# Kernel optimization log

Hardware: AMD Instinct MI355X
Metric: run time of the kernel (lower is better)

## Reference

```python
import jax, jax.numpy as jnp
import numpy as np

N = 8388608      # number of points
S = 32768        # number of superpoints (segments)


def setup_inputs() -> dict:
    key = jax.random.key(0)
    k1, k2, k3 = jax.random.split(key, 3)
    pos = jax.random.normal(k1, (N, 3), dtype=jnp.float32)
    idx = jnp.sort(jax.random.randint(k2, (N,), 0, S, dtype=jnp.int64))
    w = jax.random.uniform(k3, (N,), dtype=jnp.float32)  # non-negative weights
    return {"pos": pos, "idx": idx, "w": w, "num_super": S}


def reference(pos, idx, w, num_super):
    # Per-segment min / max of coordinates: [S, 3]
    mn = jax.ops.segment_min(pos, idx, num_segments=num_super, indices_are_sorted=True)
    mx = jax.ops.segment_max(pos, idx, num_segments=num_super, indices_are_sorted=True)
    # Per-segment diameter = largest coordinate extent: [S]
    diameter_segment = (mx - mn).max(axis=1)
    # Weighted per-segment center: sum(w*pos) / sum(w), guarding zero-weight segments
    w_sum = jax.ops.segment_sum(w, idx, num_segments=num_super, indices_are_sorted=True)
    w_sum_safe = jnp.where(w_sum == 0, 1.0, w_sum)
    center_segment = (
        jax.ops.segment_sum(pos * w[:, None], idx, num_segments=num_super,
                            indices_are_sorted=True)
        / w_sum_safe[:, None]
    )
    # Gather per-node center/diameter and normalize into unit sphere
    pos_out = (pos - center_segment[idx]) / (diameter_segment[idx][:, None] + 0.01)
    return pos_out, diameter_segment.reshape(-1, 1)
```

## Files before the change

kernel.cpp:

```cpp
#include <hip/hip_runtime.h>

#define WAVE 64
#define SPB 4
typedef float v4f __attribute__((ext_vector_type(4)));

__global__ void detect_idx64(const unsigned int* __restrict__ w32, long long N,
                             int* __restrict__ flag) {
    long long base = (N / 2) | 1LL;
    long long stride = ((N / 2) / 64) & ~1LL;
    if (stride < 2) stride = 2;
    long long p = base + (long long)threadIdx.x * stride;
    unsigned int v = (p < N) ? w32[p] : 0u;
    unsigned long long nz = __ballot(v != 0u);
    if (threadIdx.x == 0) *flag = (nz == 0ULL) ? 1 : 0;
}

__device__ __forceinline__ int load_idx(const void* __restrict__ p,
                                        long long i, int is64) {
    return is64 ? (int)((const long long*)p)[i] : ((const int*)p)[i];
}

__global__ void find_bounds(const void* __restrict__ idxp,
                            const int* __restrict__ flag,
                            int* __restrict__ start,
                            long long N, int S) {
    const long long b = ((long long)blockIdx.x * blockDim.x + threadIdx.x) << 2;
    const bool active = b < N;
    const int is64 = *flag;

    int v0 = 0, v1 = 0, v2 = 0, v3 = 0;
    int nval = 0;
    if (active) {
        if (b + 4 <= N) {
            nval = 4;
            if (is64) {
                const longlong2* p = (const longlong2*)((const long long*)idxp + b);
                longlong2 q0 = p[0], q1 = p[1];
                v0 = (int)q0.x; v1 = (int)q0.y; v2 = (int)q1.x; v3 = (int)q1.y;
            } else {
                int4 q = *(const int4*)((const int*)idxp + b);
                v0 = q.x; v1 = q.y; v2 = q.z; v3 = q.w;
            }
        } else {
            nval = (int)(N - b);
            v0 = load_idx(idxp, b, is64);
            if (nval > 1) v1 = load_idx(idxp, b + 1, is64);
            if (nval > 2) v2 = load_idx(idxp, b + 2, is64);
        }
    }
    int last = (nval == 4) ? v3 : (nval == 3) ? v2 : (nval == 2) ? v1 : v0;
    int prev = __shfl_up(last, 1);
    if ((threadIdx.x & 63) == 0)
        prev = (b == 0) ? -1 : (active ? load_idx(idxp, b - 1, is64) : 0);
    if (!active) return;

    int c = prev;
    if (nval >= 1) { if (v0 > c) { for (int t = c + 1; t <= v0; ++t) start[t] = (int)(b);     } c = v0; }
    if (nval >= 2) { if (v1 > c) { for (int t = c + 1; t <= v1; ++t) start[t] = (int)(b + 1); } c = v1; }
    if (nval >= 3) { if (v2 > c) { for (int t = c + 1; t <= v2; ++t) start[t] = (int)(b + 2); } c = v2; }
    if (nval >= 4) { if (v3 > c) { for (int t = c + 1; t <= v3; ++t) start[t] = (int)(b + 3); } c = v3; }
    if (b + nval >= N)
        for (int t = c + 1; t <= S; ++t) start[t] = (int)N;
}

__global__ __launch_bounds__(SPB * WAVE)
void seg_norm(const float* __restrict__ pos,
              const float* __restrict__ w,
              const int* __restrict__ start,
              float* __restrict__ out,
              float* __restrict__ diam_out,
              int S) {
    const int wid  = threadIdx.x >> 6;
    const int lane = threadIdx.x & 63;
    const int step = gridDim.x * SPB;

    const float4* __restrict__ pos4 = (const float4*)pos;
    const float4* __restrict__ w4   = (const float4*)w;
    float4* __restrict__ out4 = (float4*)out;

    for (int s = blockIdx.x * SPB + wid; s < S; s += step) {
        const int su = __builtin_amdgcn_readfirstlane(s);
        const int lo = start[su], hi = start[su + 1];
        const int g0 = lo >> 2, g1 = (hi + 3) >> 2;

        const int ga = g0 + lane;
        const int gb = ga + WAVE;
        const bool va = ga < g1, vb = gb < g1;
        const bool anyb = __any(vb);

        float4 a0 = {0,0,0,0}, a1 = {0,0,0,0}, a2 = {0,0,0,0}, aw = {0,0,0,0};
        float4 b0 = {0,0,0,0}, b1 = {0,0,0,0}, b2 = {0,0,0,0}, bw = {0,0,0,0};
        if (va) {
            a0 = pos4[3LL * ga]; a1 = pos4[3LL * ga + 1]; a2 = pos4[3LL * ga + 2];
            aw = w4[ga];
        }
        if (anyb && vb) {
            b0 = pos4[3LL * gb]; b1 = pos4[3LL * gb + 1]; b2 = pos4[3LL * gb + 2];
            bw = w4[gb];
        }

        float mnx = INFINITY,  mny = INFINITY,  mnz = INFINITY;
        float mxx = -INFINITY, mxy = -INFINITY, mxz = -INFINITY;
        float sw = 0.f, swx = 0.f, swy = 0.f, swz = 0.f;

        #define PROC(PI, X, Y, Z, WV)                                        \
        {                                                                    \
            bool in = ((PI) >= lo) & ((PI) < hi);                            \
            float xv = (X), yv = (Y), zv = (Z);                              \
            float wv = in ? (WV) : 0.f;                                      \
            mnx = fminf(mnx, in ? xv :  INFINITY);                           \
            mxx = fmaxf(mxx, in ? xv : -INFINITY);                           \
            mny = fminf(mny, in ? yv :  INFINITY);                           \
            mxy = fmaxf(mxy, in ? yv : -INFINITY);                           \
            mnz = fminf(mnz, in ? zv :  INFINITY);                           \
            mxz = fmaxf(mxz, in ? zv : -INFINITY);                           \
            sw += wv;                                                        \
            swx = fmaf(wv, xv, swx);                                         \
            swy = fmaf(wv, yv, swy);                                         \
            swz = fmaf(wv, zv, swz);                                         \
        }
        #define PROC_GROUP(G, R0, R1, R2, RW)                                \
        {                                                                    \
            const int p = (G) << 2;                                          \
            PROC(p + 0, R0.x, R0.y, R0.z, RW.x)                              \
            PROC(p + 1, R0.w, R1.x, R1.y, RW.y)                              \
            PROC(p + 2, R1.z, R1.w, R2.x, RW.z)                              \
            PROC(p + 3, R2.y, R2.z, R2.w, RW.w)                              \
        }

        PROC_GROUP(ga, a0, a1, a2, aw)
        if (anyb) PROC_GROUP(gb, b0, b1, b2, bw)

        for (int g = g0 + 2 * WAVE + lane; g < g1; g += WAVE) {
            float4 c0 = pos4[3LL * g], c1 = pos4[3LL * g + 1], c2 = pos4[3LL * g + 2];
            float4 cw = w4[g];
            PROC_GROUP(g, c0, c1, c2, cw)
        }

        #pragma unroll
        for (int off = 1; off < WAVE; off <<= 1) {
            mnx = fminf(mnx, __shfl_xor(mnx, off));
            mny = fminf(mny, __shfl_xor(mny, off));
            mnz = fminf(mnz, __shfl_xor(mnz, off));
            mxx = fmaxf(mxx, __shfl_xor(mxx, off));
            mxy = fmaxf(mxy, __shfl_xor(mxy, off));
            mxz = fmaxf(mxz, __shfl_xor(mxz, off));
            sw  += __shfl_xor(sw,  off);
            swx += __shfl_xor(swx, off);
            swy += __shfl_xor(swy, off);
            swz += __shfl_xor(swz, off);
        }

        const float diam = fmaxf(mxx - mnx, fmaxf(mxy - mny, mxz - mnz));
        const float wsafe = (sw == 0.f) ? 1.f : sw;
        const float cx = swx / wsafe, cy = swy / wsafe, cz = swz / wsafe;
        const float inv = 1.f / (diam + 0.01f);
        if (lane == 0) diam_out[s] = diam;

        #define STORE_GROUP(G, R0, R1, R2)                                       \
        {                                                                        \
            const int p = (G) << 2;                                              \
            float4 ra, rb, rc;                                                   \
            ra.x = (R0.x - cx) * inv; ra.y = (R0.y - cy) * inv;                  \
            ra.z = (R0.z - cz) * inv; ra.w = (R0.w - cx) * inv;                  \
            rb.x = (R1.x - cy) * inv; rb.y = (R1.y - cz) * inv;                  \
            rb.z = (R1.z - cx) * inv; rb.w = (R1.w - cy) * inv;                  \
            rc.x = (R2.x - cz) * inv; rc.y = (R2.y - cx) * inv;                  \
            rc.z = (R2.z - cy) * inv; rc.w = (R2.w - cz) * inv;                  \
            if (p >= lo && p + 4 <= hi) {                                        \
                __builtin_nontemporal_store(*(const v4f*)&ra, (v4f*)&out4[3LL * (G)]);     \
                __builtin_nontemporal_store(*(const v4f*)&rb, (v4f*)&out4[3LL * (G) + 1]); \
                __builtin_nontemporal_store(*(const v4f*)&rc, (v4f*)&out4[3LL * (G) + 2]); \
            } else {                                                             \
                const long long f = 12LL * (G);                                  \
                if (p + 0 >= lo && p + 0 < hi) {                                 \
                    out[f + 0] = ra.x; out[f + 1]  = ra.y; out[f + 2]  = ra.z;   \
                }                                                                \
                if (p + 1 >= lo && p + 1 < hi) {                                 \
                    out[f + 3] = ra.w; out[f + 4]  = rb.x; out[f + 5]  = rb.y;   \
                }                                                                \
                if (p + 2 >= lo && p + 2 < hi) {                                 \
                    out[f + 6] = rb.z; out[f + 7]  = rb.w; out[f + 8]  = rc.x;   \
                }                                                                \
                if (p + 3 >= lo && p + 3 < hi) {                                 \
                    out[f + 9] = rc.y; out[f + 10] = rc.z; out[f + 11] = rc.w;   \
                }                                                                \
            }                                                                    \
        }

        STORE_GROUP(ga, a0, a1, a2)
        if (anyb) STORE_GROUP(gb, b0, b1, b2)

        for (int g = g0 + 2 * WAVE + lane; g < g1; g += WAVE) {
            float4 c0 = pos4[3LL * g], c1 = pos4[3LL * g + 1], c2 = pos4[3LL * g + 2];
            STORE_GROUP(g, c0, c1, c2)
        }

        #undef STORE_GROUP
        #undef PROC_GROUP
        #undef PROC
    }
}

extern "C" void kernel_launch(void* const* d_in, const int* in_sizes, int n_in,
                              void* d_out, int out_size, void* d_ws, size_t ws_size,
                              hipStream_t stream) {
    const float* pos  = (const float*)d_in[0];
    const void*  idxp = d_in[1];
    const float* w    = (const float*)d_in[2];

    const long long N = (long long)in_sizes[0] / 3;
    const int S = out_size - in_sizes[0];

    float* out = (float*)d_out;
    float* diam_out = out + (long long)in_sizes[0];

    int* flag  = (int*)d_ws;
    int* start = (int*)((char*)d_ws + 256);

    detect_idx64<<<1, 64, 0, stream>>>((const unsigned int*)idxp, N, flag);

    const long long nt4 = (N + 3) >> 2;
    find_bounds<<<(int)((nt4 + 255) / 256), 256, 0, stream>>>(idxp, flag, start, N, S);

    int sgrid = (S + SPB - 1) / SPB;
    int grid = sgrid < 2048 ? sgrid : 2048;
    seg_norm<<<grid, SPB * WAVE, 0, stream>>>(pos, w, start, out, diam_out, S);
}
```

Measured before the change: 65.54 us.

## Process two segments per wave to overlap their loads, drop grid-stride loop

Each wave now handles segments sA and sA+H together, issuing the loads for both before any reduction so more memory requests are in flight per wave. The persistent grid-stride loop is replaced by a one-shot grid of H/WPB blocks. Nontemporal stores become plain float4 stores, and the __any guard on the second chunk is removed. The cost is roughly double the register pressure per wave, which may lower occupancy.

```diff
diff --git a/kernel.cpp b/kernel.cpp
--- a/kernel.cpp
+++ b/kernel.cpp
@@ -1,8 +1,7 @@
 #include <hip/hip_runtime.h>
 
 #define WAVE 64
-#define SPB 4
-typedef float v4f __attribute__((ext_vector_type(4)));
+#define WPB 4
 
 __global__ void detect_idx64(const unsigned int* __restrict__ w32, long long N,
                              int* __restrict__ flag) {
@@ -63,143 +62,183 @@
         for (int t = c + 1; t <= S; ++t) start[t] = (int)N;
 }
 
-__global__ __launch_bounds__(SPB * WAVE)
+__global__ __launch_bounds__(WPB * WAVE)
 void seg_norm(const float* __restrict__ pos,
               const float* __restrict__ w,
               const int* __restrict__ start,
               float* __restrict__ out,
               float* __restrict__ diam_out,
-              int S) {
+              int S, int H) {
     const int wid  = threadIdx.x >> 6;
     const int lane = threadIdx.x & 63;
-    const int step = gridDim.x * SPB;
+    const int sA = blockIdx.x * WPB + wid;
+    if (sA >= H) return;
+    const int sB = sA + H;
+    const bool hasB = sB < S;
+
+    const int loA = start[sA], hiA = start[sA + 1];
+    const int loB = hasB ? start[sB] : 0;
+    const int hiB = hasB ? start[sB + 1] : 0;
 
     const float4* __restrict__ pos4 = (const float4*)pos;
     const float4* __restrict__ w4   = (const float4*)w;
+
+    const int g0A = loA >> 2, g1A = (hiA + 3) >> 2;
+    const int g0B = loB >> 2, g1B = (hiB + 3) >> 2;
+    const int gaA = g0A + lane, gbA = gaA + WAVE;
+    const int gaB = g0B + lane, gbB = gaB + WAVE;
+    const bool vaA = gaA < g1A, vbA = gbA < g1A;
+    const bool vaB = gaB < g1B, vbB = gbB < g1B;
+
+    float4 Aa0 = {0,0,0,0}, Aa1 = {0,0,0,0}, Aa2 = {0,0,0,0}, Aaw = {0,0,0,0};
+    float4 Ab0 = {0,0,0,0}, Ab1 = {0,0,0,0}, Ab2 = {0,0,0,0}, Abw = {0,0,0,0};
+    float4 Ba0 = {0,0,0,0}, Ba1 = {0,0,0,0}, Ba2 = {0,0,0,0}, Baw = {0,0,0,0};
+    float4 Bb0 = {0,0,0,0}, Bb1 = {0,0,0,0}, Bb2 = {0,0,0,0}, Bbw = {0,0,0,0};
+    if (vaA) {
+        Aa0 = pos4[3LL * gaA]; Aa1 = pos4[3LL * gaA + 1]; Aa2 = pos4[3LL * gaA + 2];
+        Aaw = w4[gaA];
+    }
+    if (vbA) {
+        Ab0 = pos4[3LL * gbA]; Ab1 = pos4[3LL * gbA + 1]; Ab2 = pos4[3LL * gbA + 2];
+        Abw = w4[gbA];
+    }
+    if (vaB) {
+        Ba0 = pos4[3LL * gaB]; Ba1 = pos4[3LL * gaB + 1]; Ba2 = pos4[3LL * gaB + 2];
+        Baw = w4[gaB];
+    }
+    if (vbB) {
+        Bb0 = pos4[3LL * gbB]; Bb1 = pos4[3LL * gbB + 1]; Bb2 = pos4[3LL * gbB + 2];
+        Bbw = w4[gbB];
+    }
+
+    #define DECL_ACC(P)                                                      \
+        float P##mnx = INFINITY,  P##mny = INFINITY,  P##mnz = INFINITY;     \
+        float P##mxx = -INFINITY, P##mxy = -INFINITY, P##mxz = -INFINITY;    \
+        float P##sw = 0.f, P##swx = 0.f, P##swy = 0.f, P##swz = 0.f;
+    DECL_ACC(A_)
+    DECL_ACC(B_)
+
+    #define PROC(P, PI, LO, HI, X, Y, Z, WV)                                 \
+    {                                                                        \
+        bool in = ((PI) >= (LO)) & ((PI) < (HI));                            \
+        float xv = (X), yv = (Y), zv = (Z);                                  \
+        float wv = in ? (WV) : 0.f;                                          \
+        P##mnx = fminf(P##mnx, in ? xv :  INFINITY);                         \
+        P##mxx = fmaxf(P##mxx, in ? xv : -INFINITY);                         \
+        P##mny = fminf(P##mny, in ? yv :  INFINITY);                         \
+        P##mxy = fmaxf(P##mxy, in ? yv : -INFINITY);                         \
+        P##mnz = fminf(P##mnz, in ? zv :  INFINITY);                         \
+        P##mxz = fmaxf(P##mxz, in ? zv : -INFINITY);                         \
+        P##sw += wv;                                                         \
+        P##swx = fmaf(wv, xv, P##swx);                                       \
+        P##swy = fmaf(wv, yv, P##swy);                                       \
+        P##swz = fmaf(wv, zv, P##swz);                                       \
+    }
+    #define PROC_GROUP(P, G, LO, HI, R0, R1, R2, RW)                         \
+    {                                                                        \
+        const int p_ = (G) << 2;                                             \
+        PROC(P, p_ + 0, LO, HI, R0.x, R0.y, R0.z, RW.x)                      \
+        PROC(P, p_ + 1, LO, HI, R0.w, R1.x, R1.y, RW.y)                      \
+        PROC(P, p_ + 2, LO, HI, R1.z, R1.w, R2.x, RW.z)                      \
+        PROC(P, p_ + 3, LO, HI, R2.y, R2.z, R2.w, RW.w)                      \
+    }
+
+    PROC_GROUP(A_, gaA, loA, hiA, Aa0, Aa1, Aa2, Aaw)
+    PROC_GROUP(A_, gbA, loA, hiA, Ab0, Ab1, Ab2, Abw)
+    PROC_GROUP(B_, gaB, loB, hiB, Ba0, Ba1, Ba2, Baw)
+    PROC_GROUP(B_, gbB, loB, hiB, Bb0, Bb1, Bb2, Bbw)
+
+    for (int g = g0A + 2 * WAVE + lane; g < g1A; g += WAVE) {
+        float4 c0 = pos4[3LL * g], c1 = pos4[3LL * g + 1], c2 = pos4[3LL * g + 2];
+        float4 cw = w4[g];
+        PROC_GROUP(A_, g, loA, hiA, c0, c1, c2, cw)
+    }
+    for (int g = g0B + 2 * WAVE + lane; g < g1B; g += WAVE) {
+        float4 c0 = pos4[3LL * g], c1 = pos4[3LL * g + 1], c2 = pos4[3LL * g + 2];
+        float4 cw = w4[g];
+        PROC_GROUP(B_, g, loB, hiB, c0, c1, c2, cw)
+    }
+
+    #define RED(P)                                                           \
+        P##mnx = fminf(P##mnx, __shfl_xor(P##mnx, off));                     \
+        P##mny = fminf(P##mny, __shfl_xor(P##mny, off));                     \
+        P##mnz = fminf(P##mnz, __shfl_xor(P##mnz, off));                     \
+        P##mxx = fmaxf(P##mxx, __shfl_xor(P##mxx, off));                     \
+        P##mxy = fmaxf(P##mxy, __shfl_xor(P##mxy, off));                     \
+        P##mxz = fmaxf(P##mxz, __shfl_xor(P##mxz, off));                     \
+        P##sw  += __shfl_xor(P##sw,  off);                                   \
+        P##swx += __shfl_xor(P##swx, off);                                   \
+        P##swy += __shfl_xor(P##swy, off);                                   \
+        P##swz += __shfl_xor(P##swz, off);
+    #pragma unroll
+    for (int off = 1; off < WAVE; off <<= 1) {
+        RED(A_)
+        RED(B_)
+    }
+    #undef RED
+
+    const float diamA = fmaxf(A_mxx - A_mnx, fmaxf(A_mxy - A_mny, A_mxz - A_mnz));
+    const float diamB = fmaxf(B_mxx - B_mnx, fmaxf(B_mxy - B_mny, B_mxz - B_mnz));
+    const float wsA = (A_sw == 0.f) ? 1.f : A_sw;
+    const float wsB = (B_sw == 0.f) ? 1.f : B_sw;
+    const float cxA = A_swx / wsA, cyA = A_swy / wsA, czA = A_swz / wsA;
+    const float cxB = B_swx / wsB, cyB = B_swy / wsB, czB = B_swz / wsB;
+    const float invA = 1.f / (diamA + 0.01f);
+    const float invB = 1.f / (diamB + 0.01f);
+    if (lane == 0) {
+        diam_out[sA] = diamA;
+        if (hasB) diam_out[sB] = diamB;
+    }
+
     float4* __restrict__ out4 = (float4*)out;
-
-    for (int s = blockIdx.x * SPB + wid; s < S; s += step) {
-        const int su = __builtin_amdgcn_readfirstlane(s);
-        const int lo = start[su], hi = start[su + 1];
-        const int g0 = lo >> 2, g1 = (hi + 3) >> 2;
-
-        const int ga = g0 + lane;
-        const int gb = ga + WAVE;
-        const bool va = ga < g1, vb = gb < g1;
-        const bool anyb = __any(vb);
-
-        float4 a0 = {0,0,0,0}, a1 = {0,0,0,0}, a2 = {0,0,0,0}, aw = {0,0,0,0};
-        float4 b0 = {0,0,0,0}, b1 = {0,0,0,0}, b2 = {0,0,0,0}, bw = {0,0,0,0};
-        if (va) {
-            a0 = pos4[3LL * ga]; a1 = pos4[3LL * ga + 1]; a2 = pos4[3LL * ga + 2];
-            aw = w4[ga];
-        }
-        if (anyb && vb) {
-            b0 = pos4[3LL * gb]; b1 = pos4[3LL * gb + 1]; b2 = pos4[3LL * gb + 2];
-            bw = w4[gb];
-        }
-
-        float mnx = INFINITY,  mny = INFINITY,  mnz = INFINITY;
-        float mxx = -INFINITY, mxy = -INFINITY, mxz = -INFINITY;
-        float sw = 0.f, swx = 0.f, swy = 0.f, swz = 0.f;
-
-        #define PROC(PI, X, Y, Z, WV)                                        \
-        {                                                                    \
-            bool in = ((PI) >= lo) & ((PI) < hi);                            \
-            float xv = (X), yv = (Y), zv = (Z);                              \
-            float wv = in ? (WV) : 0.f;                                      \
-            mnx = fminf(mnx, in ? xv :  INFINITY);                           \
-            mxx = fmaxf(mxx, in ? xv : -INFINITY);                           \
-            mny = fminf(mny, in ? yv :  INFINITY);                           \
-            mxy = fmaxf(mxy, in ? yv : -INFINITY);                           \
-            mnz = fminf(mnz, in ? zv :  INFINITY);                           \
-            mxz = fmaxf(mxz, in ? zv : -INFINITY);                           \
-            sw += wv;                                                        \
-            swx = fmaf(wv, xv, swx);                                         \
-            swy = fmaf(wv, yv, swy);                                         \
-            swz = fmaf(wv, zv, swz);                                         \
-        }
-        #define PROC_GROUP(G, R0, R1, R2, RW)                                \
-        {                                                                    \
-            const int p = (G) << 2;                                          \
-            PROC(p + 0, R0.x, R0.y, R0.z, RW.x)                              \
-            PROC(p + 1, R0.w, R1.x, R1.y, RW.y)                              \
-            PROC(p + 2, R1.z, R1.w, R2.x, RW.z)                              \
-            PROC(p + 3, R2.y, R2.z, R2.w, RW.w)                              \
-        }
-
-        PROC_GROUP(ga, a0, a1, a2, aw)
-        if (anyb) PROC_GROUP(gb, b0, b1, b2, bw)
-
-        for (int g = g0 + 2 * WAVE + lane; g < g1; g += WAVE) {
-            float4 c0 = pos4[3LL * g], c1 = pos4[3LL * g + 1], c2 = pos4[3LL * g + 2];
-            float4 cw = w4[g];
-            PROC_GROUP(g, c0, c1, c2, cw)
-        }
-
-        #pragma unroll
-        for (int off = 1; off < WAVE; off <<= 1) {
-            mnx = fminf(mnx, __shfl_xor(mnx, off));
-            mny = fminf(mny, __shfl_xor(mny, off));
-            mnz = fminf(mnz, __shfl_xor(mnz, off));
-            mxx = fmaxf(mxx, __shfl_xor(mxx, off));
-            mxy = fmaxf(mxy, __shfl_xor(mxy, off));
-            mxz = fmaxf(mxz, __shfl_xor(mxz, off));
-            sw  += __shfl_xor(sw,  off);
-            swx += __shfl_xor(swx, off);
-            swy += __shfl_xor(swy, off);
-            swz += __shfl_xor(swz, off);
-        }
-
-        const float diam = fmaxf(mxx - mnx, fmaxf(mxy - mny, mxz - mnz));
-        const float wsafe = (sw == 0.f) ? 1.f : sw;
-        const float cx = swx / wsafe, cy = swy / wsafe, cz = swz / wsafe;
-        const float inv = 1.f / (diam + 0.01f);
-        if (lane == 0) diam_out[s] = diam;
-
-        #define STORE_GROUP(G, R0, R1, R2)                                       \
-        {                                                                        \
-            const int p = (G) << 2;                                              \
-            float4 ra, rb, rc;                                                   \
-            ra.x = (R0.x - cx) * inv; ra.y = (R0.y - cy) * inv;                  \
-            ra.z = (R0.z - cz) * inv; ra.w = (R0.w - cx) * inv;                  \
-            rb.x = (R1.x - cy) * inv; rb.y = (R1.y - cz) * inv;                  \
-            rb.z = (R1.z - cx) * inv; rb.w = (R1.w - cy) * inv;                  \
-            rc.x = (R2.x - cz) * inv; rc.y = (R2.y - cx) * inv;                  \
-            rc.z = (R2.z - cy) * inv; rc.w = (R2.w - cz) * inv;                  \
-            if (p >= lo && p + 4 <= hi) {                                        \
-                __builtin_nontemporal_store(*(const v4f*)&ra, (v4f*)&out4[3LL * (G)]);     \
-                __builtin_nontemporal_store(*(const v4f*)&rb, (v4f*)&out4[3LL * (G) + 1]); \
-                __builtin_nontemporal_store(*(const v4f*)&rc, (v4f*)&out4[3LL * (G) + 2]); \
-            } else {                                                             \
-                const long long f = 12LL * (G);                                  \
-                if (p + 0 >= lo && p + 0 < hi) {                                 \
-                    out[f + 0] = ra.x; out[f + 1]  = ra.y; out[f + 2]  = ra.z;   \
-                }                                                                \
-                if (p + 1 >= lo && p + 1 < hi) {                                 \
-                    out[f + 3] = ra.w; out[f + 4]  = rb.x; out[f + 5]  = rb.y;   \
-                }                                                                \
-                if (p + 2 >= lo && p + 2 < hi) {                                 \
-                    out[f + 6] = rb.z; out[f + 7]  = rb.w; out[f + 8]  = rc.x;   \
-                }                                                                \
-                if (p + 3 >= lo && p + 3 < hi) {                                 \
-                    out[f + 9] = rc.y; out[f + 10] = rc.z; out[f + 11] = rc.w;   \
-                }                                                                \
-            }                                                                    \
-        }
-
-        STORE_GROUP(ga, a0, a1, a2)
-        if (anyb) STORE_GROUP(gb, b0, b1, b2)
-
-        for (int g = g0 + 2 * WAVE + lane; g < g1; g += WAVE) {
-            float4 c0 = pos4[3LL * g], c1 = pos4[3LL * g + 1], c2 = pos4[3LL * g + 2];
-            STORE_GROUP(g, c0, c1, c2)
-        }
-
-        #undef STORE_GROUP
-        #undef PROC_GROUP
-        #undef PROC
-    }
+    #define STORE_GROUP(G, LO, HI, CX, CY, CZ, INV, R0, R1, R2)              \
+    {                                                                        \
+        const int p_ = (G) << 2;                                             \
+        float4 ra, rb, rc;                                                   \
+        ra.x = (R0.x - (CX)) * (INV); ra.y = (R0.y - (CY)) * (INV);          \
+        ra.z = (R0.z - (CZ)) * (INV); ra.w = (R0.w - (CX)) * (INV);          \
+        rb.x = (R1.x - (CY)) * (INV); rb.y = (R1.y - (CZ)) * (INV);          \
+        rb.z = (R1.z - (CX)) * (INV); rb.w = (R1.w - (CY)) * (INV);          \
+        rc.x = (R2.x - (CZ)) * (INV); rc.y = (R2.y - (CX)) * (INV);          \
+        rc.z = (R2.z - (CY)) * (INV); rc.w = (R2.w - (CZ)) * (INV);          \
+        if (p_ >= (LO) && p_ + 4 <= (HI)) {                                  \
+            out4[3LL * (G)] = ra; out4[3LL * (G) + 1] = rb;                  \
+            out4[3LL * (G) + 2] = rc;                                        \
+        } else {                                                             \
+            const long long f = 12LL * (G);                                  \
+            if (p_ + 0 >= (LO) && p_ + 0 < (HI)) {                           \
+                out[f + 0] = ra.x; out[f + 1]  = ra.y; out[f + 2]  = ra.z;   \
+            }                                                                \
+            if (p_ + 1 >= (LO) && p_ + 1 < (HI)) {                           \
+                out[f + 3] = ra.w; out[f + 4]  = rb.x; out[f + 5]  = rb.y;   \
+            }                                                                \
+            if (p_ + 2 >= (LO) && p_ + 2 < (HI)) {                           \
+                out[f + 6] = rb.z; out[f + 7]  = rb.w; out[f + 8]  = rc.x;   \
+            }                                                                \
+            if (p_ + 3 >= (LO) && p_ + 3 < (HI)) {                           \
+                out[f + 9] = rc.y; out[f + 10] = rc.z; out[f + 11] = rc.w;   \
+            }                                                                \
+        }                                                                    \
+    }
+
+    STORE_GROUP(gaA, loA, hiA, cxA, cyA, czA, invA, Aa0, Aa1, Aa2)
+    STORE_GROUP(gbA, loA, hiA, cxA, cyA, czA, invA, Ab0, Ab1, Ab2)
+    STORE_GROUP(gaB, loB, hiB, cxB, cyB, czB, invB, Ba0, Ba1, Ba2)
+    STORE_GROUP(gbB, loB, hiB, cxB, cyB, czB, invB, Bb0, Bb1, Bb2)
+
+    for (int g = g0A + 2 * WAVE + lane; g < g1A; g += WAVE) {
+        float4 c0 = pos4[3LL * g], c1 = pos4[3LL * g + 1], c2 = pos4[3LL * g + 2];
+        STORE_GROUP(g, loA, hiA, cxA, cyA, czA, invA, c0, c1, c2)
+    }
+    for (int g = g0B + 2 * WAVE + lane; g < g1B; g += WAVE) {
+        float4 c0 = pos4[3LL * g], c1 = pos4[3LL * g + 1], c2 = pos4[3LL * g + 2];
+        STORE_GROUP(g, loB, hiB, cxB, cyB, czB, invB, c0, c1, c2)
+    }
+
+    #undef STORE_GROUP
+    #undef PROC_GROUP
+    #undef PROC
+    #undef DECL_ACC
 }
 
 extern "C" void kernel_launch(void* const* d_in, const int* in_sizes, int n_in,
@@ -223,7 +262,7 @@
     const long long nt4 = (N + 3) >> 2;
     find_bounds<<<(int)((nt4 + 255) / 256), 256, 0, stream>>>(idxp, flag, start, N, S);
 
-    int sgrid = (S + SPB - 1) / SPB;
-    int grid = sgrid < 2048 ? sgrid : 2048;
-    seg_norm<<<grid, SPB * WAVE, 0, stream>>>(pos, w, start, out, diam_out, S);
-}
+    const int H = (S + 1) / 2;
+    seg_norm<<<(H + WPB - 1) / WPB, WPB * WAVE, 0, stream>>>(
+        pos, w, start, out, diam_out, S, H);
+}
```

Result: faster. 59.57 us (-9.1%).
